# Kernel optimization log

Hardware: AMD Instinct MI355X
Metric: run time of the kernel (lower is better)

The kernel has to match this reference:

```python
import jax, jax.numpy as jnp
import numpy as np

SIGMA = 1.0

def setup_inputs() -> dict:
    key = jax.random.key(0)
    k1, k2 = jax.random.split(key)
    N, IN, OUT = 524288, 64, 128
    x = jax.random.normal(k1, (N, IN), dtype=jnp.float32)
    bin_centers = jax.random.normal(k2, (OUT, IN), dtype=jnp.float32)
    return {"x": x, "bin_centers": bin_centers}

def reference(x, bin_centers):
    # distances[n,o] = sum_i (x[n,i] - c[o,i])^2 = ||x_n||^2 - 2 x_n.c_o + ||c_o||^2
    x2 = jnp.sum(x * x, axis=1)[:, None]                # [N,1]
    c2 = jnp.sum(bin_centers * bin_centers, axis=1)[None, :]  # [1,O]
    xc = jnp.einsum('ni,oi->no', x, bin_centers)        # [N,O] GEMM
    distances = x2 - 2.0 * xc + c2                      # [N,O]
    rbf = jnp.exp(-distances / (2.0 * SIGMA ** 2))      # [N,O]
    # histogram[o,i] = sum_n rbf[n,o] * x[n,i]  ->  rbf^T @ x
    histogram = jnp.einsum('no,ni->oi', rbf, x)         # [O,I] GEMM
    return histogram
```

## Files before the change

kernel.cpp:

```cpp
#include <hip/hip_runtime.h>
#include <stdint.h>


typedef _Float16 half8v __attribute__((ext_vector_type(8)));
typedef _Float16 half4v __attribute__((ext_vector_type(4)));
typedef __fp16  fp16x2 __attribute__((ext_vector_type(2)));
typedef float floatx4 __attribute__((ext_vector_type(4)));

#define GRIDN 1024
#define NITER 16
#define LOG2E 1.4426950408889634f
#define PBIAS 38.0f
#define PUNSCALE 3.637978807091713e-12f

#if __has_builtin(__builtin_amdgcn_exp2f)
#define EXP2F(x) __builtin_amdgcn_exp2f(x)
#else
#define EXP2F(x) exp2f(x)
#endif

static __device__ __forceinline__ unsigned int pk16z(float a, float b) {
  fp16x2 h = __builtin_amdgcn_cvt_pkrtz(a, b);
  return __builtin_bit_cast(unsigned int, h);
}
static __device__ __forceinline__ unsigned int pk16(float a, float b) {
  unsigned short ha = __builtin_bit_cast(unsigned short, (_Float16)a);
  unsigned short hb = __builtin_bit_cast(unsigned short, (_Float16)b);
  return (unsigned int)ha | ((unsigned int)hb << 16);
}
static __device__ __forceinline__ half4v mkh4(unsigned int lo, unsigned int hi) {
  uint2 u{lo, hi};
  return __builtin_bit_cast(half4v, u);
}
static __device__ __forceinline__ half8v mkh8(unsigned int a, unsigned int b,
                                              unsigned int c, unsigned int d) {
  uint4 u{a, b, c, d};
  return __builtin_bit_cast(half8v, u);
}

static __device__ __forceinline__ floatx4 mfma32(half8v a, half8v b, floatx4 c) {
  return __builtin_amdgcn_mfma_f32_16x16x32_f16(a, b, c, 0, 0, 0);
}
static __device__ __forceinline__ floatx4 mfma16(half4v a, half4v b, floatx4 c) {
  return __builtin_amdgcn_mfma_f32_16x16x16f16(a, b, c, 0, 0, 0);
}

#define LSTR 72

__global__ __launch_bounds__(128, 2) void rbf_hist_kernel(
    const float* __restrict__ x, const float* __restrict__ c,
    float* __restrict__ out, float* __restrict__ ws, int use_ws) {
  __shared__ unsigned short sXh[32][LSTR];
  __shared__ float          sX2[32];

  const int t    = threadIdx.x;
  const int lane = t & 63;
  const int w    = t >> 6;
  const int l15  = lane & 15;
  const int quad = lane >> 4;

  half8v chi[4][2], clo[4][2];
  float m2c[4];
#pragma unroll
  for (int oo = 0; oo < 4; ++oo) {
    const int ot = 4 * w + oo;
    float sq = 0.f;
#pragma unroll
    for (int s = 0; s < 2; ++s) {
      const float* p = c + (ot * 16 + l15) * 64 + s * 32 + quad * 8;
      float4 va = *(const float4*)(p);
      float4 vb = *(const float4*)(p + 4);
      float f[8] = {va.x, va.y, va.z, va.w, vb.x, vb.y, vb.z, vb.w};
      unsigned int h[4], l[4];
#pragma unroll
      for (int jp = 0; jp < 4; ++jp) {
        float a = f[2 * jp], b = f[2 * jp + 1];
        sq = fmaf(a, a, sq);
        sq = fmaf(b, b, sq);
        a *= LOG2E; b *= LOG2E;
        unsigned int hp = pk16(a, b);
        float ha = (float)__builtin_bit_cast(_Float16, (unsigned short)(hp & 0xffffu));
        float hb = (float)__builtin_bit_cast(_Float16, (unsigned short)(hp >> 16));
        h[jp] = hp;
        l[jp] = pk16z(a - ha, b - hb);
      }
      chi[oo][s] = mkh8(h[0], h[1], h[2], h[3]);
      clo[oo][s] = mkh8(l[0], l[1], l[2], l[3]);
    }
    sq += __shfl_xor(sq, 16);
    sq += __shfl_xor(sq, 32);
    m2c[oo] = fmaf(-0.5f * LOG2E, sq, PBIAS);
  }

  half4v iden;
  {
    float e0 = (quad * 4 + 0 == l15) ? 1.f : 0.f;
    float e1 = (quad * 4 + 1 == l15) ? 1.f : 0.f;
    float e2 = (quad * 4 + 2 == l15) ? 1.f : 0.f;
    float e3 = (quad * 4 + 3 == l15) ? 1.f : 0.f;
    iden = mkh4(pk16z(e0, e1), pk16z(e2, e3));
  }

  floatx4 hacc[4][4];
#pragma unroll
  for (int a = 0; a < 4; ++a)
#pragma unroll
    for (int b = 0; b < 4; ++b) {
      floatx4 z = {0.f, 0.f, 0.f, 0.f};
      hacc[a][b] = z;
    }

  const int r = t >> 2, q = t & 3;
  float4 v[4];
  {
    const size_t row0 = (size_t)(blockIdx.x * 32 + r) * 64 + q * 16;
#pragma unroll
    for (int u = 0; u < 4; ++u)
      v[u] = *(const float4*)(x + row0 + u * 4);
  }

  for (int it = 0; it < NITER; ++it) {
    __syncthreads();

    {
      float sq = 0.f;
      unsigned int hw[8];
#pragma unroll
      for (int u = 0; u < 4; ++u) {
        float f0 = v[u].x, f1 = v[u].y, f2 = v[u].z, f3 = v[u].w;
        sq = fmaf(f0, f0, sq); sq = fmaf(f1, f1, sq);
        sq = fmaf(f2, f2, sq); sq = fmaf(f3, f3, sq);
        hw[2 * u]     = pk16(f0, f1);
        hw[2 * u + 1] = pk16(f2, f3);
      }
      *(uint4*)&sXh[r][q * 16]     = uint4{hw[0], hw[1], hw[2], hw[3]};
      *(uint4*)&sXh[r][q * 16 + 8] = uint4{hw[4], hw[5], hw[6], hw[7]};
      sq += __shfl_xor(sq, 1);
      sq += __shfl_xor(sq, 2);
      if (q == 0) sX2[r] = -0.5f * LOG2E * sq;
    }
    __syncthreads();

    if (it < NITER - 1) {
      const size_t nrow =
          (size_t)((blockIdx.x + (it + 1) * GRIDN) * 32 + r) * 64 + q * 16;
#pragma unroll
      for (int u = 0; u < 4; ++u)
        v[u] = *(const float4*)(x + nrow + u * 4);
    }

    half4v P[4][2];
#pragma unroll
    for (int t2 = 0; t2 < 2; ++t2) {
      half8v xh0 = *(const half8v*)&sXh[t2 * 16 + l15][quad * 8];
      half8v xh1 = *(const half8v*)&sXh[t2 * 16 + l15][32 + quad * 8];
      float4 m2x = *(const float4*)&sX2[t2 * 16 + quad * 4];
#pragma unroll
      for (int oo = 0; oo < 4; ++oo) {
        floatx4 accA = {m2x.x + m2c[oo], m2x.y + m2c[oo],
                        m2x.z + m2c[oo], m2x.w + m2c[oo]};
        floatx4 accB = {0.f, 0.f, 0.f, 0.f};
        accA = mfma32(xh0, chi[oo][0], accA);
        accB = mfma32(xh1, clo[oo][1], accB);
        accA = mfma32(xh1, chi[oo][1], accA);
        accB = mfma32(xh0, clo[oo][0], accB);
        floatx4 acc = accA + accB;
        P[oo][t2] = mkh4(pk16(EXP2F(acc[0]), EXP2F(acc[1])),
                         pk16(EXP2F(acc[2]), EXP2F(acc[3])));
      }
    }

    half4v XT[4][2];
#pragma unroll
    for (int t2 = 0; t2 < 2; ++t2)
#pragma unroll
      for (int itl = 0; itl < 4; ++itl) {
        half4v ax = *(const half4v*)&sXh[t2 * 16 + l15][itl * 16 + quad * 4];
        floatx4 z = {0.f, 0.f, 0.f, 0.f};
        floatx4 d = mfma16(ax, iden, z);
        XT[itl][t2] = mkh4(pk16z(d[0], d[1]), pk16z(d[2], d[3]));
      }

#pragma unroll
    for (int t2 = 0; t2 < 2; ++t2)
#pragma unroll
      for (int oo = 0; oo < 4; ++oo)
#pragma unroll
        for (int itl = 0; itl < 4; ++itl)
          hacc[oo][itl] = mfma16(P[oo][t2], XT[itl][t2], hacc[oo][itl]);
  }

  if (use_ws) {
    float* part = ws + (size_t)blockIdx.x * 8192;
#pragma unroll
    for (int oo = 0; oo < 4; ++oo)
#pragma unroll
      for (int itl = 0; itl < 4; ++itl)
#pragma unroll
        for (int e = 0; e < 4; ++e) {
          int o = (4 * w + oo) * 16 + quad * 4 + e;
          int i = itl * 16 + l15;
          part[o * 64 + i] = hacc[oo][itl][e] * PUNSCALE;
        }
  } else {
#pragma unroll
    for (int oo = 0; oo < 4; ++oo)
#pragma unroll
      for (int itl = 0; itl < 4; ++itl)
#pragma unroll
        for (int e = 0; e < 4; ++e) {
          int o = (4 * w + oo) * 16 + quad * 4 + e;
          int i = itl * 16 + l15;
          atomicAdd(out + o * 64 + i, hacc[oo][itl][e] * PUNSCALE);
        }
  }
}

__global__ void reduce_kernel(const float* __restrict__ ws, float* __restrict__ out) {
  const int tid = blockIdx.x * 256 + threadIdx.x;
  const int e = tid & 8191;
  const int part = tid >> 13;
  const float* p = ws + (size_t)part * 256 * 8192 + e;
  float s = 0.f;
#pragma unroll 8
  for (int b = 0; b < 256; ++b) s += p[(size_t)b * 8192];
  atomicAdd(out + e, s);
}

__global__ void zero_out_kernel(float* out, int n) {
  int i = blockIdx.x * 256 + threadIdx.x;
  if (i < n) out[i] = 0.f;
}

extern "C" void kernel_launch(void* const* d_in, const int* in_sizes, int n_in,
                              void* d_out, int out_size, void* d_ws, size_t ws_size,
                              hipStream_t stream) {
  (void)in_sizes; (void)n_in;
  const float* x = (const float*)d_in[0];
  const float* c = (const float*)d_in[1];
  float* out = (float*)d_out;
  float* ws  = (float*)d_ws;

  const int use_ws = (ws_size >= (size_t)GRIDN * 8192 * sizeof(float)) ? 1 : 0;

  zero_out_kernel<<<(out_size + 255) / 256, 256, 0, stream>>>(out, out_size);
  rbf_hist_kernel<<<GRIDN, 128, 0, stream>>>(x, c, out, ws, use_ws);
  if (use_ws)
    reduce_kernel<<<128, 256, 0, stream>>>(ws, out);
}
```

Baseline: 207.3 us.

## Give each wave private x rows, drop block barriers, and store the reduce result directly

The block is restructured to 256 threads (4 waves) working on 16 rows per iteration. Each wave loads its own x rows straight into MFMA operand registers and handles 2 of the 8 output tiles instead of 4. Block-wide barriers and the shared x-norm buffer go away: the norm is reduced with shuffles, and shared memory is used only for each wave's private transpose staging. The reduce kernel now sums all 1024 partials per element with 32 blocks and writes the output directly, removing the zero-fill kernel and the atomics. The risks are that every wave now recomputes the same x norms and conversions, and that the single-pass reduce has little parallelism.

```diff
diff --git a/kernel.cpp b/kernel.cpp
--- a/kernel.cpp
+++ b/kernel.cpp
@@ -8,7 +8,7 @@
 typedef float floatx4 __attribute__((ext_vector_type(4)));
 
 #define GRIDN 1024
-#define NITER 16
+#define NITER 32
 #define LOG2E 1.4426950408889634f
 #define PBIAS 38.0f
 #define PUNSCALE 3.637978807091713e-12f
@@ -47,11 +47,10 @@
 
 #define LSTR 72
 
-__global__ __launch_bounds__(128, 2) void rbf_hist_kernel(
+__global__ __launch_bounds__(256, 3) void rbf_hist_kernel(
     const float* __restrict__ x, const float* __restrict__ c,
     float* __restrict__ out, float* __restrict__ ws, int use_ws) {
-  __shared__ unsigned short sXh[32][LSTR];
-  __shared__ float          sX2[32];
+  __shared__ unsigned short sT[4][16][LSTR];
 
   const int t    = threadIdx.x;
   const int lane = t & 63;
@@ -59,11 +58,11 @@
   const int l15  = lane & 15;
   const int quad = lane >> 4;
 
-  half8v chi[4][2], clo[4][2];
-  float m2c[4];
-#pragma unroll
-  for (int oo = 0; oo < 4; ++oo) {
-    const int ot = 4 * w + oo;
+  half8v chi[2][2], clo[2][2];
+  float m2c[2];
+#pragma unroll
+  for (int oo = 0; oo < 2; ++oo) {
+    const int ot = 2 * w + oo;
     float sq = 0.f;
 #pragma unroll
     for (int s = 0; s < 2; ++s) {
@@ -101,130 +100,121 @@
     iden = mkh4(pk16z(e0, e1), pk16z(e2, e3));
   }
 
-  floatx4 hacc[4][4];
-#pragma unroll
-  for (int a = 0; a < 4; ++a)
+  floatx4 hacc[2][4];
+#pragma unroll
+  for (int a = 0; a < 2; ++a)
 #pragma unroll
     for (int b = 0; b < 4; ++b) {
       floatx4 z = {0.f, 0.f, 0.f, 0.f};
       hacc[a][b] = z;
     }
 
-  const int r = t >> 2, q = t & 3;
   float4 v[4];
   {
-    const size_t row0 = (size_t)(blockIdx.x * 32 + r) * 64 + q * 16;
-#pragma unroll
-    for (int u = 0; u < 4; ++u)
-      v[u] = *(const float4*)(x + row0 + u * 4);
+    const float* rp = x + ((size_t)blockIdx.x * 16 + l15) * 64;
+    v[0] = *(const float4*)(rp + quad * 8);
+    v[1] = *(const float4*)(rp + quad * 8 + 4);
+    v[2] = *(const float4*)(rp + 32 + quad * 8);
+    v[3] = *(const float4*)(rp + 32 + quad * 8 + 4);
   }
 
   for (int it = 0; it < NITER; ++it) {
-    __syncthreads();
-
-    {
-      float sq = 0.f;
-      unsigned int hw[8];
-#pragma unroll
-      for (int u = 0; u < 4; ++u) {
-        float f0 = v[u].x, f1 = v[u].y, f2 = v[u].z, f3 = v[u].w;
-        sq = fmaf(f0, f0, sq); sq = fmaf(f1, f1, sq);
-        sq = fmaf(f2, f2, sq); sq = fmaf(f3, f3, sq);
-        hw[2 * u]     = pk16(f0, f1);
-        hw[2 * u + 1] = pk16(f2, f3);
-      }
-      *(uint4*)&sXh[r][q * 16]     = uint4{hw[0], hw[1], hw[2], hw[3]};
-      *(uint4*)&sXh[r][q * 16 + 8] = uint4{hw[4], hw[5], hw[6], hw[7]};
-      sq += __shfl_xor(sq, 1);
-      sq += __shfl_xor(sq, 2);
-      if (q == 0) sX2[r] = -0.5f * LOG2E * sq;
-    }
-    __syncthreads();
+    float sq = 0.f;
+#pragma unroll
+    for (int u = 0; u < 4; ++u) {
+      sq = fmaf(v[u].x, v[u].x, sq);
+      sq = fmaf(v[u].y, v[u].y, sq);
+      sq = fmaf(v[u].z, v[u].z, sq);
+      sq = fmaf(v[u].w, v[u].w, sq);
+    }
+    half8v xh0 = mkh8(pk16(v[0].x, v[0].y), pk16(v[0].z, v[0].w),
+                      pk16(v[1].x, v[1].y), pk16(v[1].z, v[1].w));
+    half8v xh1 = mkh8(pk16(v[2].x, v[2].y), pk16(v[2].z, v[2].w),
+                      pk16(v[3].x, v[3].y), pk16(v[3].z, v[3].w));
+
+    *(uint4*)&sT[w][l15][quad * 8]      = __builtin_bit_cast(uint4, xh0);
+    *(uint4*)&sT[w][l15][32 + quad * 8] = __builtin_bit_cast(uint4, xh1);
 
     if (it < NITER - 1) {
-      const size_t nrow =
-          (size_t)((blockIdx.x + (it + 1) * GRIDN) * 32 + r) * 64 + q * 16;
-#pragma unroll
-      for (int u = 0; u < 4; ++u)
-        v[u] = *(const float4*)(x + nrow + u * 4);
-    }
-
-    half4v P[4][2];
-#pragma unroll
-    for (int t2 = 0; t2 < 2; ++t2) {
-      half8v xh0 = *(const half8v*)&sXh[t2 * 16 + l15][quad * 8];
-      half8v xh1 = *(const half8v*)&sXh[t2 * 16 + l15][32 + quad * 8];
-      float4 m2x = *(const float4*)&sX2[t2 * 16 + quad * 4];
-#pragma unroll
-      for (int oo = 0; oo < 4; ++oo) {
-        floatx4 accA = {m2x.x + m2c[oo], m2x.y + m2c[oo],
-                        m2x.z + m2c[oo], m2x.w + m2c[oo]};
-        floatx4 accB = {0.f, 0.f, 0.f, 0.f};
-        accA = mfma32(xh0, chi[oo][0], accA);
-        accB = mfma32(xh1, clo[oo][1], accB);
-        accA = mfma32(xh1, chi[oo][1], accA);
-        accB = mfma32(xh0, clo[oo][0], accB);
-        floatx4 acc = accA + accB;
-        P[oo][t2] = mkh4(pk16(EXP2F(acc[0]), EXP2F(acc[1])),
-                         pk16(EXP2F(acc[2]), EXP2F(acc[3])));
-      }
-    }
-
-    half4v XT[4][2];
-#pragma unroll
-    for (int t2 = 0; t2 < 2; ++t2)
-#pragma unroll
-      for (int itl = 0; itl < 4; ++itl) {
-        half4v ax = *(const half4v*)&sXh[t2 * 16 + l15][itl * 16 + quad * 4];
-        floatx4 z = {0.f, 0.f, 0.f, 0.f};
-        floatx4 d = mfma16(ax, iden, z);
-        XT[itl][t2] = mkh4(pk16z(d[0], d[1]), pk16z(d[2], d[3]));
-      }
-
-#pragma unroll
-    for (int t2 = 0; t2 < 2; ++t2)
-#pragma unroll
-      for (int oo = 0; oo < 4; ++oo)
-#pragma unroll
-        for (int itl = 0; itl < 4; ++itl)
-          hacc[oo][itl] = mfma16(P[oo][t2], XT[itl][t2], hacc[oo][itl]);
+      const float* np =
+          x + ((size_t)(blockIdx.x + (it + 1) * GRIDN) * 16 + l15) * 64;
+      v[0] = *(const float4*)(np + quad * 8);
+      v[1] = *(const float4*)(np + quad * 8 + 4);
+      v[2] = *(const float4*)(np + 32 + quad * 8);
+      v[3] = *(const float4*)(np + 32 + quad * 8 + 4);
+    }
+
+    sq += __shfl_xor(sq, 16);
+    sq += __shfl_xor(sq, 32);
+    float m2x[4];
+#pragma unroll
+    for (int e = 0; e < 4; ++e)
+      m2x[e] = -0.5f * LOG2E * __shfl(sq, quad * 4 + e);
+
+    half4v P[2];
+#pragma unroll
+    for (int oo = 0; oo < 2; ++oo) {
+      floatx4 accA = {m2x[0] + m2c[oo], m2x[1] + m2c[oo],
+                      m2x[2] + m2c[oo], m2x[3] + m2c[oo]};
+      floatx4 accB = {0.f, 0.f, 0.f, 0.f};
+      accA = mfma32(xh0, chi[oo][0], accA);
+      accB = mfma32(xh1, clo[oo][1], accB);
+      accA = mfma32(xh1, chi[oo][1], accA);
+      accB = mfma32(xh0, clo[oo][0], accB);
+      floatx4 acc = accA + accB;
+      P[oo] = mkh4(pk16(EXP2F(acc[0]), EXP2F(acc[1])),
+                   pk16(EXP2F(acc[2]), EXP2F(acc[3])));
+    }
+
+    half4v XT[4];
+#pragma unroll
+    for (int itl = 0; itl < 4; ++itl) {
+      half4v ax = *(const half4v*)&sT[w][l15][itl * 16 + quad * 4];
+      floatx4 z = {0.f, 0.f, 0.f, 0.f};
+      floatx4 d = mfma16(ax, iden, z);
+      XT[itl] = mkh4(pk16z(d[0], d[1]), pk16z(d[2], d[3]));
+    }
+
+#pragma unroll
+    for (int oo = 0; oo < 2; ++oo)
+#pragma unroll
+      for (int itl = 0; itl < 4; ++itl)
+        hacc[oo][itl] = mfma16(P[oo], XT[itl], hacc[oo][itl]);
   }
 
   if (use_ws) {
     float* part = ws + (size_t)blockIdx.x * 8192;
 #pragma unroll
-    for (int oo = 0; oo < 4; ++oo)
+    for (int oo = 0; oo < 2; ++oo)
 #pragma unroll
       for (int itl = 0; itl < 4; ++itl)
 #pragma unroll
         for (int e = 0; e < 4; ++e) {
-          int o = (4 * w + oo) * 16 + quad * 4 + e;
+          int o = (2 * w + oo) * 16 + quad * 4 + e;
           int i = itl * 16 + l15;
           part[o * 64 + i] = hacc[oo][itl][e] * PUNSCALE;
         }
   } else {
 #pragma unroll
-    for (int oo = 0; oo < 4; ++oo)
+    for (int oo = 0; oo < 2; ++oo)
 #pragma unroll
       for (int itl = 0; itl < 4; ++itl)
 #pragma unroll
         for (int e = 0; e < 4; ++e) {
-          int o = (4 * w + oo) * 16 + quad * 4 + e;
+          int o = (2 * w + oo) * 16 + quad * 4 + e;
           int i = itl * 16 + l15;
           atomicAdd(out + o * 64 + i, hacc[oo][itl][e] * PUNSCALE);
         }
   }
 }
 
-__global__ void reduce_kernel(const float* __restrict__ ws, float* __restrict__ out) {
-  const int tid = blockIdx.x * 256 + threadIdx.x;
-  const int e = tid & 8191;
-  const int part = tid >> 13;
-  const float* p = ws + (size_t)part * 256 * 8192 + e;
+__global__ void reduce_store_kernel(const float* __restrict__ ws,
+                                    float* __restrict__ out) {
+  const int e = blockIdx.x * 256 + threadIdx.x;
   float s = 0.f;
 #pragma unroll 8
-  for (int b = 0; b < 256; ++b) s += p[(size_t)b * 8192];
-  atomicAdd(out + e, s);
+  for (int b = 0; b < GRIDN; ++b) s += ws[(size_t)b * 8192 + e];
+  out[e] = s;
 }
 
 __global__ void zero_out_kernel(float* out, int n) {
@@ -243,8 +233,11 @@
 
   const int use_ws = (ws_size >= (size_t)GRIDN * 8192 * sizeof(float)) ? 1 : 0;
 
-  zero_out_kernel<<<(out_size + 255) / 256, 256, 0, stream>>>(out, out_size);
-  rbf_hist_kernel<<<GRIDN, 128, 0, stream>>>(x, c, out, ws, use_ws);
-  if (use_ws)
-    reduce_kernel<<<128, 256, 0, stream>>>(ws, out);
-}
+  if (use_ws) {
+    rbf_hist_kernel<<<GRIDN, 256, 0, stream>>>(x, c, out, ws, 1);
+    reduce_store_kernel<<<32, 256, 0, stream>>>(ws, out);
+  } else {
+    zero_out_kernel<<<(out_size + 255) / 256, 256, 0, stream>>>(out, out_size);
+    rbf_hist_kernel<<<GRIDN, 256, 0, stream>>>(x, c, out, ws, 0);
+  }
+}
```

Result: slower. 248.2 us (+19.7%).

## Drop hi/lo fp16 split for centers and restructure into 256-thread blocks

Applied to the files above, without the earlier changes.

Removes the compensated low-part fp16 term for the scaled bin centers, halving the MFMAs in the distance GEMM. Blocks grow to four waves, each owning two output tiles, with the grid doubled and iterations per block halved to reduce register pressure and raise occupancy. The per-block partial workspace and the reduction launch double in size, adding write/read traffic. Losing the low-part term reduces accuracy of the exponent argument.

```diff
diff --git a/kernel.cpp b/kernel.cpp
--- a/kernel.cpp
+++ b/kernel.cpp
@@ -7,8 +7,8 @@
 typedef __fp16  fp16x2 __attribute__((ext_vector_type(2)));
 typedef float floatx4 __attribute__((ext_vector_type(4)));
 
-#define GRIDN 1024
-#define NITER 16
+#define GRIDN 2048
+#define NITER 8
 #define LOG2E 1.4426950408889634f
 #define PBIAS 38.0f
 #define PUNSCALE 3.637978807091713e-12f
@@ -47,7 +47,7 @@
 
 #define LSTR 72
 
-__global__ __launch_bounds__(128, 2) void rbf_hist_kernel(
+__global__ __launch_bounds__(256, 4) void rbf_hist_kernel(
     const float* __restrict__ x, const float* __restrict__ c,
     float* __restrict__ out, float* __restrict__ ws, int use_ws) {
   __shared__ unsigned short sXh[32][LSTR];
@@ -59,11 +59,11 @@
   const int l15  = lane & 15;
   const int quad = lane >> 4;
 
-  half8v chi[4][2], clo[4][2];
-  float m2c[4];
-#pragma unroll
-  for (int oo = 0; oo < 4; ++oo) {
-    const int ot = 4 * w + oo;
+  half8v chi[2][2];
+  float m2c[2];
+#pragma unroll
+  for (int oo = 0; oo < 2; ++oo) {
+    const int ot = 2 * w + oo;
     float sq = 0.f;
 #pragma unroll
     for (int s = 0; s < 2; ++s) {
@@ -71,21 +71,15 @@
       float4 va = *(const float4*)(p);
       float4 vb = *(const float4*)(p + 4);
       float f[8] = {va.x, va.y, va.z, va.w, vb.x, vb.y, vb.z, vb.w};
-      unsigned int h[4], l[4];
+      unsigned int h[4];
 #pragma unroll
       for (int jp = 0; jp < 4; ++jp) {
         float a = f[2 * jp], b = f[2 * jp + 1];
         sq = fmaf(a, a, sq);
         sq = fmaf(b, b, sq);
-        a *= LOG2E; b *= LOG2E;
-        unsigned int hp = pk16(a, b);
-        float ha = (float)__builtin_bit_cast(_Float16, (unsigned short)(hp & 0xffffu));
-        float hb = (float)__builtin_bit_cast(_Float16, (unsigned short)(hp >> 16));
-        h[jp] = hp;
-        l[jp] = pk16z(a - ha, b - hb);
+        h[jp] = pk16(a * LOG2E, b * LOG2E);
       }
       chi[oo][s] = mkh8(h[0], h[1], h[2], h[3]);
-      clo[oo][s] = mkh8(l[0], l[1], l[2], l[3]);
     }
     sq += __shfl_xor(sq, 16);
     sq += __shfl_xor(sq, 32);
@@ -101,115 +95,104 @@
     iden = mkh4(pk16z(e0, e1), pk16z(e2, e3));
   }
 
-  floatx4 hacc[4][4];
-#pragma unroll
-  for (int a = 0; a < 4; ++a)
+  floatx4 hacc[2][4];
+#pragma unroll
+  for (int a = 0; a < 2; ++a)
 #pragma unroll
     for (int b = 0; b < 4; ++b) {
       floatx4 z = {0.f, 0.f, 0.f, 0.f};
       hacc[a][b] = z;
     }
 
-  const int r = t >> 2, q = t & 3;
-  float4 v[4];
+  const int r = t >> 3, q = t & 7;
+  float4 v[2];
   {
-    const size_t row0 = (size_t)(blockIdx.x * 32 + r) * 64 + q * 16;
-#pragma unroll
-    for (int u = 0; u < 4; ++u)
-      v[u] = *(const float4*)(x + row0 + u * 4);
+    const float* p = x + ((size_t)blockIdx.x * 32 + r) * 64 + q * 8;
+    v[0] = *(const float4*)(p);
+    v[1] = *(const float4*)(p + 4);
   }
 
   for (int it = 0; it < NITER; ++it) {
     __syncthreads();
 
     {
+      float f0 = v[0].x, f1 = v[0].y, f2 = v[0].z, f3 = v[0].w;
+      float f4 = v[1].x, f5 = v[1].y, f6 = v[1].z, f7 = v[1].w;
       float sq = 0.f;
-      unsigned int hw[8];
-#pragma unroll
-      for (int u = 0; u < 4; ++u) {
-        float f0 = v[u].x, f1 = v[u].y, f2 = v[u].z, f3 = v[u].w;
-        sq = fmaf(f0, f0, sq); sq = fmaf(f1, f1, sq);
-        sq = fmaf(f2, f2, sq); sq = fmaf(f3, f3, sq);
-        hw[2 * u]     = pk16(f0, f1);
-        hw[2 * u + 1] = pk16(f2, f3);
-      }
-      *(uint4*)&sXh[r][q * 16]     = uint4{hw[0], hw[1], hw[2], hw[3]};
-      *(uint4*)&sXh[r][q * 16 + 8] = uint4{hw[4], hw[5], hw[6], hw[7]};
+      sq = fmaf(f0, f0, sq); sq = fmaf(f1, f1, sq);
+      sq = fmaf(f2, f2, sq); sq = fmaf(f3, f3, sq);
+      sq = fmaf(f4, f4, sq); sq = fmaf(f5, f5, sq);
+      sq = fmaf(f6, f6, sq); sq = fmaf(f7, f7, sq);
+      *(uint4*)&sXh[r][q * 8] =
+          uint4{pk16(f0, f1), pk16(f2, f3), pk16(f4, f5), pk16(f6, f7)};
       sq += __shfl_xor(sq, 1);
       sq += __shfl_xor(sq, 2);
+      sq += __shfl_xor(sq, 4);
       if (q == 0) sX2[r] = -0.5f * LOG2E * sq;
     }
     __syncthreads();
 
     if (it < NITER - 1) {
-      const size_t nrow =
-          (size_t)((blockIdx.x + (it + 1) * GRIDN) * 32 + r) * 64 + q * 16;
-#pragma unroll
-      for (int u = 0; u < 4; ++u)
-        v[u] = *(const float4*)(x + nrow + u * 4);
-    }
-
-    half4v P[4][2];
+      const float* p =
+          x + ((size_t)(blockIdx.x + (it + 1) * GRIDN) * 32 + r) * 64 + q * 8;
+      v[0] = *(const float4*)(p);
+      v[1] = *(const float4*)(p + 4);
+    }
+
 #pragma unroll
     for (int t2 = 0; t2 < 2; ++t2) {
       half8v xh0 = *(const half8v*)&sXh[t2 * 16 + l15][quad * 8];
       half8v xh1 = *(const half8v*)&sXh[t2 * 16 + l15][32 + quad * 8];
       float4 m2x = *(const float4*)&sX2[t2 * 16 + quad * 4];
-#pragma unroll
-      for (int oo = 0; oo < 4; ++oo) {
-        floatx4 accA = {m2x.x + m2c[oo], m2x.y + m2c[oo],
-                        m2x.z + m2c[oo], m2x.w + m2c[oo]};
-        floatx4 accB = {0.f, 0.f, 0.f, 0.f};
-        accA = mfma32(xh0, chi[oo][0], accA);
-        accB = mfma32(xh1, clo[oo][1], accB);
-        accA = mfma32(xh1, chi[oo][1], accA);
-        accB = mfma32(xh0, clo[oo][0], accB);
-        floatx4 acc = accA + accB;
-        P[oo][t2] = mkh4(pk16(EXP2F(acc[0]), EXP2F(acc[1])),
-                         pk16(EXP2F(acc[2]), EXP2F(acc[3])));
+
+      half4v P[2];
+#pragma unroll
+      for (int oo = 0; oo < 2; ++oo) {
+        floatx4 acc = {m2x.x + m2c[oo], m2x.y + m2c[oo],
+                       m2x.z + m2c[oo], m2x.w + m2c[oo]};
+        acc = mfma32(xh0, chi[oo][0], acc);
+        acc = mfma32(xh1, chi[oo][1], acc);
+        P[oo] = mkh4(pk16(EXP2F(acc[0]), EXP2F(acc[1])),
+                     pk16(EXP2F(acc[2]), EXP2F(acc[3])));
       }
-    }
-
-    half4v XT[4][2];
-#pragma unroll
-    for (int t2 = 0; t2 < 2; ++t2)
+
+      half4v XT[4];
 #pragma unroll
       for (int itl = 0; itl < 4; ++itl) {
         half4v ax = *(const half4v*)&sXh[t2 * 16 + l15][itl * 16 + quad * 4];
         floatx4 z = {0.f, 0.f, 0.f, 0.f};
         floatx4 d = mfma16(ax, iden, z);
-        XT[itl][t2] = mkh4(pk16z(d[0], d[1]), pk16z(d[2], d[3]));
+        XT[itl] = mkh4(pk16z(d[0], d[1]), pk16z(d[2], d[3]));
       }
 
 #pragma unroll
-    for (int t2 = 0; t2 < 2; ++t2)
-#pragma unroll
-      for (int oo = 0; oo < 4; ++oo)
+      for (int oo = 0; oo < 2; ++oo)
 #pragma unroll
         for (int itl = 0; itl < 4; ++itl)
-          hacc[oo][itl] = mfma16(P[oo][t2], XT[itl][t2], hacc[oo][itl]);
+          hacc[oo][itl] = mfma16(P[oo], XT[itl], hacc[oo][itl]);
+    }
   }
 
   if (use_ws) {
     float* part = ws + (size_t)blockIdx.x * 8192;
 #pragma unroll
-    for (int oo = 0; oo < 4; ++oo)
+    for (int oo = 0; oo < 2; ++oo)
 #pragma unroll
       for (int itl = 0; itl < 4; ++itl)
 #pragma unroll
         for (int e = 0; e < 4; ++e) {
-          int o = (4 * w + oo) * 16 + quad * 4 + e;
+          int o = (2 * w + oo) * 16 + quad * 4 + e;
           int i = itl * 16 + l15;
           part[o * 64 + i] = hacc[oo][itl][e] * PUNSCALE;
         }
   } else {
 #pragma unroll
-    for (int oo = 0; oo < 4; ++oo)
+    for (int oo = 0; oo < 2; ++oo)
 #pragma unroll
       for (int itl = 0; itl < 4; ++itl)
 #pragma unroll
         for (int e = 0; e < 4; ++e) {
-          int o = (4 * w + oo) * 16 + quad * 4 + e;
+          int o = (2 * w + oo) * 16 + quad * 4 + e;
           int i = itl * 16 + l15;
           atomicAdd(out + o * 64 + i, hacc[oo][itl][e] * PUNSCALE);
         }
@@ -244,7 +227,7 @@
   const int use_ws = (ws_size >= (size_t)GRIDN * 8192 * sizeof(float)) ? 1 : 0;
 
   zero_out_kernel<<<(out_size + 255) / 256, 256, 0, stream>>>(out, out_size);
-  rbf_hist_kernel<<<GRIDN, 128, 0, stream>>>(x, c, out, ws, use_ws);
+  rbf_hist_kernel<<<GRIDN, 256, 0, stream>>>(x, c, out, ws, use_ws);
   if (use_ws)
-    reduce_kernel<<<128, 256, 0, stream>>>(ws, out);
-}
+    reduce_kernel<<<256, 256, 0, stream>>>(ws, out);
+}
```

New measurement: 217.2 us. +4.7%, slower.
